# Performance work log

Measured on AMD Instinct MI355X. Metric: run time of the kernel, lower is better.

## Reference

```python
import jax, jax.numpy as jnp
import numpy as np

EPS_LN = 1e-6
NUM_HEADS = 3

def ln2d(x, w, b):
    # channels-first layernorm over dim 1 (biased variance), matching LayerNormFunction
    mu = x.mean(1, keepdims=True)
    var = ((x - mu) ** 2).mean(1, keepdims=True)
    y = (x - mu) * jax.lax.rsqrt(var + EPS_LN)
    return w[None, :, None, None] * y + b[None, :, None, None]

def conv1x1(x, w, b):
    # w: (out, in)
    return jnp.einsum('bchw,oc->bohw', x, w) + b[None, :, None, None]

def dwconv3x3(x, w, b):
    # w: (C,1,3,3), depthwise
    C = x.shape[1]
    y = jax.lax.conv_general_dilated(x, w, (1, 1), 'SAME',
        feature_group_count=C, dimension_numbers=('NCHW', 'OIHW', 'NCHW'))
    return y + b[None, :, None, None]

def l2norm(x, eps=1e-12):
    n = jnp.sqrt(jnp.sum(x * x, axis=-1, keepdims=True))
    return x / jnp.maximum(n, eps)

def forward(x, ln1_w, ln1_b, qkv_w, qkv_b, dw_w, dw_b, temp,
            ca_w1, ca_b1, ca_w2, ca_b2, beta, beta2,
            ln2_w, ln2_b, conv4_w, conv4_b, conv5_w, conv5_b, gamma):
    inp = x
    b, c, h, w = x.shape
    xn = ln2d(x, ln1_w, ln1_b)

    # CAB = SE channel attention
    y = xn.mean(axis=(2, 3), keepdims=True)                      # (b,c,1,1)
    y = jax.nn.relu(conv1x1(y, ca_w1, ca_b1))
    y = jax.nn.sigmoid(conv1x1(y, ca_w2, ca_b2))
    outc = xn * y

    # QKV
    qkv = dwconv3x3(conv1x1(xn, qkv_w, qkv_b), dw_w, dw_b)       # (b,3c,h,w)
    q, k, v = jnp.split(qkv, 3, axis=1)
    cph = c // NUM_HEADS
    def to_tokens(t):  # (b,c,h,w) -> (b,head,hw,cph)
        return t.reshape(b, NUM_HEADS, cph, h * w).transpose(0, 1, 3, 2)
    qs = l2norm(to_tokens(q))
    ks = l2norm(to_tokens(k))
    vs = to_tokens(v)

    attns = jnp.einsum('bhnc,bhmc->bhnm', qs, ks) * temp[None]   # (b,head,hw,hw)
    attns = jax.nn.softmax(jax.nn.relu(attns), axis=-1)
    outs = jnp.einsum('bhnm,bhmc->bhnc', attns, vs)              # (b,head,hw,cph)
    outs = outs.transpose(0, 1, 3, 2).reshape(b, c, h, w)

    y1 = inp + outc * beta + outs * beta2

    # gated conv FFN
    f = conv1x1(ln2d(y1, ln2_w, ln2_b), conv4_w, conv4_b)        # (b,2c,h,w)
    f1, f2 = jnp.split(f, 2, axis=1)
    f = conv1x1(f1 * f2, conv5_w, conv5_b)
    return y1 + f * gamma

def setup_inputs() -> dict:
    key = jax.random.key(0)
    ks = jax.random.split(key, 16)
    B, C, H, W = 2, 48, 64, 64
    r = C // 16
    s = 0.05
    return {
        'x': jax.random.normal(ks[0], (B, C, H, W), jnp.float32),
        'ln1_w': jnp.ones((C,), jnp.float32),
        'ln1_b': jnp.zeros((C,), jnp.float32),
        'qkv_w': jax.random.normal(ks[1], (3 * C, C), jnp.float32) * s,
        'qkv_b': jnp.zeros((3 * C,), jnp.float32),
        'dw_w': jax.random.normal(ks[2], (3 * C, 1, 3, 3), jnp.float32) * s,
        'dw_b': jnp.zeros((3 * C,), jnp.float32),
        'temp': jnp.ones((3, 1, 1), jnp.float32),
        'ca_w1': jax.random.normal(ks[3], (r, C), jnp.float32) * s,
        'ca_b1': jnp.zeros((r,), jnp.float32),
        'ca_w2': jax.random.normal(ks[4], (C, r), jnp.float32) * s,
        'ca_b2': jnp.zeros((C,), jnp.float32),
        'beta': jax.random.normal(ks[5], (1, C, 1, 1), jnp.float32) * 0.1,
        'beta2': jax.random.normal(ks[6], (1, C, 1, 1), jnp.float32) * 0.1,
        'ln2_w': jnp.ones((C,), jnp.float32),
        'ln2_b': jnp.zeros((C,), jnp.float32),
        'conv4_w': jax.random.normal(ks[7], (2 * C, C), jnp.float32) * s,
        'conv4_b': jnp.zeros((2 * C,), jnp.float32),
        'conv5_w': jax.random.normal(ks[8], (C, C), jnp.float32) * s,
        'conv5_b': jnp.zeros((C,), jnp.float32),
        'gamma': jax.random.normal(ks[9], (1, C, 1, 1), jnp.float32) * 0.1,
    }

def reference(x, ln1_w, ln1_b, qkv_w, qkv_b, dw_w, dw_b, temp,
              ca_w1, ca_b1, ca_w2, ca_b2, beta, beta2,
              ln2_w, ln2_b, conv4_w, conv4_b, conv5_w, conv5_b, gamma):
    return forward(x, ln1_w, ln1_b, qkv_w, qkv_b, dw_w, dw_b, temp,
                   ca_w1, ca_b1, ca_w2, ca_b2, beta, beta2,
                   ln2_w, ln2_b, conv4_w, conv4_b, conv5_w, conv5_b, gamma)
```

## Files before the change

kernel.cpp:

```cpp
#include <hip/hip_runtime.h>
#include <cstddef>
#include <cmath>

#define BN 2
#define CH 48
#define HW 4096
#define NH 3
#define QC 144
#define RR 3
#define KSPLIT 4
#define NPLANE 17
#define LOG2E 1.4426950408889634f

typedef __attribute__((ext_vector_type(8))) short bf16x8;
typedef __attribute__((ext_vector_type(16))) float f32x16;
typedef __attribute__((ext_vector_type(4))) float f32x4;

constexpr size_t OFF_BP  = 0;
constexpr size_t OFF_QB  = 12288;
constexpr size_t OFF_KB  = OFF_QB + 98304;
constexpr size_t OFF_VT  = OFF_KB + 98304;
constexpr size_t OFF_PART= OFF_VT + 98304 + 1179648;

static __device__ __forceinline__ unsigned cvtpk(float lo, float hi) {
  unsigned r;
  asm("v_cvt_pk_bf16_f32 %0, %1, %2" : "=v"(r) : "v"(lo), "v"(hi));
  return r;
}

static __device__ __forceinline__ float fexp2(float x) {
#if __has_builtin(__builtin_amdgcn_exp2f)
  return __builtin_amdgcn_exp2f(x);
#else
  float r; asm("v_exp_f32 %0, %1" : "=v"(r) : "v"(x)); return r;
#endif
}

__global__ __launch_bounds__(512) void k_front(const float* __restrict__ x,
                                               const float* __restrict__ lw,
                                               const float* __restrict__ lb,
                                               const float* __restrict__ w,
                                               const float* __restrict__ bias,
                                               const float* __restrict__ dww,
                                               const float* __restrict__ dwb,
                                               const float* __restrict__ temp,
                                               ushort* __restrict__ Qb,
                                               ushort* __restrict__ Kb,
                                               ushort* __restrict__ Vtb,
                                               float* __restrict__ bpool) {
  __shared__ float qt[3][CH][64];
  __shared__ float red1[8][64], red2[8][64];
  int blk = blockIdx.x;
  int row = blk & 63, bh = blk >> 6;
  int b = bh / NH, h = bh % NH;
  int t = threadIdx.x;
  int px = t & 63, grp = t >> 6;
  int lo = grp*18, hi = lo + 18;

  float xn[CH];
#pragma unroll
  for (int r = 0; r < 3; ++r) {
    int rlo = r*48, rhi = rlo + 48;
    if (lo >= rhi || hi <= rlo) continue;
    int yy = row + r - 1;
    bool oob = (yy < 0) || (yy >= 64);
    if (!oob) {
      const float* xb = x + (size_t)b*CH*HW + yy*64 + px;
      float s = 0.f, ss = 0.f;
#pragma unroll
      for (int ci = 0; ci < CH; ++ci) {
        float vv = xb[(size_t)ci*HW];
        xn[ci] = vv; s += vv; ss += vv*vv;
      }
      float mu = s * (1.f/CH);
      float rs2 = rsqrtf(ss*(1.f/CH) - mu*mu + 1e-6f);
#pragma unroll
      for (int ci = 0; ci < CH; ++ci)
        xn[ci] = lw[ci]*((xn[ci]-mu)*rs2) + lb[ci];
    }
    int ub = lo > rlo ? lo : rlo;
    int ue = hi < rhi ? hi : rhi;
    for (int u = ub; u < ue; ++u) {
      int oc = u - rlo;
      if (oob) { qt[r][oc][px] = 0.f; continue; }
      int c = __builtin_amdgcn_readfirstlane((oc >> 4)*48 + h*16 + (oc & 15));
      const float* wrow = w + (size_t)c*CH;
      float a = bias[c];
#pragma unroll
      for (int ci = 0; ci < CH; ++ci) a += wrow[ci]*xn[ci];
      qt[r][oc][px] = a;
    }
  }

  if (h == 0 && grp == 3) {
#pragma unroll
    for (int c = 0; c < CH; ++c) {
      float s = xn[c];
      s += __shfl_xor(s, 1);  s += __shfl_xor(s, 2);  s += __shfl_xor(s, 4);
      s += __shfl_xor(s, 8);  s += __shfl_xor(s, 16); s += __shfl_xor(s, 32);
      if (px == 0) bpool[(size_t)(b*64 + row)*CH + c] = s;
    }
  }
  __syncthreads();

  int n = row*64 + px;
  float q[2], k[2], vv2[2];
  float sq = 0.f, sk = 0.f;
#pragma unroll
  for (int j = 0; j < 2; ++j) {
    int cc = grp*2 + j;
#pragma unroll
    for (int which = 0; which < 3; ++which) {
      int oc = which*16 + cc;
      int cg = __builtin_amdgcn_readfirstlane(which*48 + h*16 + cc);
      const float* wc = dww + (size_t)cg*9;
      float w0 = wc[0], w1 = wc[1], w2 = wc[2],
            w3 = wc[3], w4 = wc[4], w5 = wc[5],
            w6 = wc[6], w7 = wc[7], w8 = wc[8];
      float a = dwb[cg];
#pragma unroll
      for (int rr = 0; rr < 3; ++rr) {
        float wl = rr==0?w0:(rr==1?w3:w6);
        float wm = rr==0?w1:(rr==1?w4:w7);
        float wr = rr==0?w2:(rr==1?w5:w8);
        float tm = qt[rr][oc][px];
        float tl = (px >= 1)  ? qt[rr][oc][px-1] : 0.f;
        float tr = (px <= 62) ? qt[rr][oc][px+1] : 0.f;
        a += wl*tl + wm*tm + wr*tr;
      }
      if (which == 0)      { q[j] = a;  sq += a*a; }
      else if (which == 1) { k[j] = a;  sk += a*a; }
      else                 vv2[j] = a;
    }
  }
  red1[grp][px] = sq; red2[grp][px] = sk;
  __syncthreads();
  float tsq = 0.f, tsk = 0.f;
#pragma unroll
  for (int i = 0; i < 8; ++i) { tsq += red1[i][px]; tsk += red2[i][px]; }
  float tq = temp[h] * LOG2E / fmaxf(sqrtf(tsq), 1e-12f);
  float ik = 1.f            / fmaxf(sqrtf(tsk), 1e-12f);
  *(uint*)(Qb + ((size_t)bh*HW + n)*16 + grp*2) = cvtpk(q[0]*tq, q[1]*tq);
  *(uint*)(Kb + ((size_t)bh*HW + n)*16 + grp*2) = cvtpk(k[0]*ik, k[1]*ik);
  Vtb[((size_t)bh*16 + grp*2    )*HW + n] = (ushort)(cvtpk(vv2[0], vv2[0]) & 0xffffu);
  Vtb[((size_t)bh*16 + grp*2 + 1)*HW + n] = (ushort)(cvtpk(vv2[1], vv2[1]) & 0xffffu);
}

#define PACK(stv, wbp) do {                                              \
  _Pragma("unroll")                                                      \
  for (int g4 = 0; g4 < 4; ++g4) {                                       \
    float e0 = fmaxf(fexp2((stv)[4*g4+0]), 1.f);                         \
    float e1 = fmaxf(fexp2((stv)[4*g4+1]), 1.f);                         \
    float e2 = fmaxf(fexp2((stv)[4*g4+2]), 1.f);                         \
    float e3 = fmaxf(fexp2((stv)[4*g4+3]), 1.f);                         \
    uint2 pk;                                                            \
    pk.x = cvtpk(e0, e1);                                                \
    pk.y = cvtpk(e2, e3);                                                \
    *(uint2*)((wbp) + wroff + 16*(g4 ^ sw)) = pk;                        \
  } } while (0)

__global__ __launch_bounds__(256) void k_attn(const ushort* __restrict__ Qb,
                                              const ushort* __restrict__ Kb,
                                              const ushort* __restrict__ Vtb,
                                              float* __restrict__ part) {
  __shared__ char smem[4][4096];
  int blk = blockIdx.x;
  int ks = blk & (KSPLIT-1);
  int qt = (blk >> 2) & 31;
  int bh = blk >> 7;
  int lane = threadIdx.x & 63;
  int wid  = threadIdx.x >> 6;
  int l31 = lane & 31;
  int lhi = lane >> 5;
  int qbase = qt*128 + wid*32;

  bf16x8 qf = *(const bf16x8*)(Qb + ((size_t)bh*HW + qbase + l31)*16 + lhi*8);

  const f32x16 z16 = {0,0,0,0,0,0,0,0,0,0,0,0,0,0,0,0};
  const short oneb = (short)0x3f80;
  const bf16x8 ones = {oneb,oneb,oneb,oneb,oneb,oneb,oneb,oneb};
  f32x4 acc0 = {0,0,0,0}, acc1 = {0,0,0,0};
  f32x4 accD0 = {0,0,0,0}, accD1 = {0,0,0,0};
  char* base = &smem[wid][0];
  int qr = lane & 15, gr = lane >> 4;
  int rdoff0 = qr*64 + 16*(gr ^ ((qr>>1)&3));
  int sw = (l31 >> 1) & 3;
  int wroff = l31*64 + 8*lhi;

  const ushort* Kbase = Kb + (size_t)bh*HW*16;
  const ushort* Vbase = Vtb + ((size_t)bh*16 + qr)*HW;
  int kbeg = ks * (HW/KSPLIT);
  constexpr int ITERS = (HW/KSPLIT)/32;

  bf16x8 kf = *(const bf16x8*)(Kbase + (size_t)(kbeg + l31)*16 + lhi*8);
  f32x16 st = __builtin_amdgcn_mfma_f32_32x32x16_bf16(kf, qf, z16, 0, 0, 0);
  bf16x8 kfn = *(const bf16x8*)(Kbase + (size_t)(kbeg + 32 + l31)*16 + lhi*8);
  bf16x8 vfn = *(const bf16x8*)(Vbase + kbeg + 8*gr);
  PACK(st, base);

#pragma unroll 4
  for (int i = 1; i < ITERS; ++i) {
    char* rb = base + ((i-1) & 1)*2048;
    bf16x8 pa0 = *(const bf16x8*)(rb + rdoff0);
    bf16x8 pa1 = *(const bf16x8*)(rb + 1024 + rdoff0);
    __builtin_amdgcn_s_setprio(1);
    f32x16 stn = __builtin_amdgcn_mfma_f32_32x32x16_bf16(kfn, qf, z16, 0, 0, 0);
    kfn = *(const bf16x8*)(Kbase + (size_t)(kbeg + (i+1)*32 + l31)*16 + lhi*8);
    bf16x8 vf = vfn;
    vfn = *(const bf16x8*)(Vbase + kbeg + i*32 + 8*gr);
    acc0  = __builtin_amdgcn_mfma_f32_16x16x32_bf16(pa0, vf, acc0, 0, 0, 0);
    acc1  = __builtin_amdgcn_mfma_f32_16x16x32_bf16(pa1, vf, acc1, 0, 0, 0);
    accD0 = __builtin_amdgcn_mfma_f32_16x16x32_bf16(pa0, ones, accD0, 0, 0, 0);
    accD1 = __builtin_amdgcn_mfma_f32_16x16x32_bf16(pa1, ones, accD1, 0, 0, 0);
    __builtin_amdgcn_s_setprio(0);
    PACK(stn, base + (i & 1)*2048);
  }
  {
    char* rb = base + ((ITERS-1) & 1)*2048;
    bf16x8 pa0 = *(const bf16x8*)(rb + rdoff0);
    bf16x8 pa1 = *(const bf16x8*)(rb + 1024 + rdoff0);
    acc0  = __builtin_amdgcn_mfma_f32_16x16x32_bf16(pa0, vfn, acc0, 0, 0, 0);
    acc1  = __builtin_amdgcn_mfma_f32_16x16x32_bf16(pa1, vfn, acc1, 0, 0, 0);
    accD0 = __builtin_amdgcn_mfma_f32_16x16x32_bf16(pa0, ones, accD0, 0, 0, 0);
    accD1 = __builtin_amdgcn_mfma_f32_16x16x32_bf16(pa1, ones, accD1, 0, 0, 0);
  }

  float* ep = (float*)base;
#pragma unroll
  for (int r = 0; r < 4; ++r) {
    ep[qr*32 + gr*4 + r]      = acc0[r];
    ep[qr*32 + gr*4 + 16 + r] = acc1[r];
  }
  if (qr == 0) {
#pragma unroll
    for (int r = 0; r < 4; ++r) {
      ep[16*32 + gr*4 + r]      = accD0[r];
      ep[16*32 + gr*4 + 16 + r] = accD1[r];
    }
  }
  __syncthreads();
  size_t pb = ((size_t)(ks*6 + bh))*NPLANE;
  for (int i = threadIdx.x; i < 4*32*NPLANE; i += 256) {
    int w = i / (32*NPLANE);
    int rem = i - w*(32*NPLANE);
    int cc = rem >> 5;
    int q = rem & 31;
    part[(pb + cc)*HW + qt*128 + w*32 + q] = ((float*)&smem[w][0])[cc*32 + q];
  }
}

__global__ __launch_bounds__(768) void k_tail(const float* __restrict__ part,
                                              const float* __restrict__ x,
                                              const float* __restrict__ lw1,
                                              const float* __restrict__ lb1,
                                              const float* __restrict__ bpool,
                                              const float* __restrict__ w1,
                                              const float* __restrict__ b1,
                                              const float* __restrict__ w2,
                                              const float* __restrict__ b2,
                                              const float* __restrict__ beta,
                                              const float* __restrict__ beta2,
                                              const float* __restrict__ lw2,
                                              const float* __restrict__ lb2,
                                              const float* __restrict__ w4,
                                              const float* __restrict__ b4,
                                              const float* __restrict__ w5,
                                              const float* __restrict__ b5,
                                              const float* __restrict__ gamma,
                                              float* __restrict__ out) {
  __shared__ float sepm[CH][4];
  __shared__ float pmL[CH];
  __shared__ float yrL[4];
  __shared__ float seL[CH];
  __shared__ float r1[12][64], r2[12][64], r3[12][64], r4[12][64];
  __shared__ float xt[CH][65];
  __shared__ float gt[CH][65];
  int t = threadIdx.x;
  int px = t & 63, w = t >> 6;
  int h = w >> 2;
  int c0 = __builtin_amdgcn_readfirstlane(w * 4);
  int qoff = __builtin_amdgcn_readfirstlane((w & 3) * 4);
  int gp = blockIdx.x*64 + px;
  int b = gp >> 12, n = gp & 4095;
  int bh = b*NH + h;

  if (t < 192) {
    int c = t % CH, j = t / CH;
    const float* bp = bpool + (size_t)(b*64 + j*16)*CH + c;
    float a = 0.f;
#pragma unroll
    for (int i = 0; i < 16; ++i) a += bp[(size_t)i*CH];
    sepm[c][j] = a;
  }
  __syncthreads();
  if (t < CH) pmL[t] = (sepm[t][0]+sepm[t][1]+sepm[t][2]+sepm[t][3]) * (1.f/HW);
  __syncthreads();
  if (t < RR) {
    float a = b1[t];
    for (int c = 0; c < CH; ++c) a += w1[t*CH+c]*pmL[c];
    yrL[t] = fmaxf(a, 0.f);
  }
  __syncthreads();
  if (t < CH) {
    float a = b2[t];
    for (int r = 0; r < RR; ++r) a += w2[t*RR+r]*yrL[r];
    seL[t] = 1.f/(1.f+__expf(-a));
  }

  float acc[4] = {0,0,0,0};
  float den = 0.f;
#pragma unroll
  for (int ks = 0; ks < KSPLIT; ++ks) {
    const float* pl = part + ((size_t)((ks*6+bh)*NPLANE + qoff))*HW + n;
#pragma unroll
    for (int cc = 0; cc < 4; ++cc) acc[cc] += pl[(size_t)cc*HW];
    den += pl[(size_t)(16 - qoff)*HW];
  }
  const float* xp = x + ((size_t)b*CH + c0)*HW + n;
  float xv[4]; float s = 0.f, ssum = 0.f;
#pragma unroll
  for (int cc = 0; cc < 4; ++cc) {
    float vv = xp[(size_t)cc*HW];
    xv[cc] = vv; s += vv; ssum += vv*vv;
  }
  r1[w][px] = s; r2[w][px] = ssum;
  __syncthreads();
  float stot = 0.f, sstot = 0.f;
#pragma unroll
  for (int i = 0; i < 12; ++i) { stot += r1[i][px]; sstot += r2[i][px]; }
  float mu = stot*(1.f/CH);
  float rs = rsqrtf(sstot*(1.f/CH) - mu*mu + 1e-6f);
  float inv = 1.f / den;
  float yv[4]; float s2 = 0.f, ss2 = 0.f;
#pragma unroll
  for (int cc = 0; cc < 4; ++cc) {
    int c = c0 + cc;
    float xnv = lw1[c]*((xv[cc]-mu)*rs) + lb1[c];
    float y = xv[cc] + xnv*seL[c]*beta[c] + acc[cc]*inv*beta2[c];
    yv[cc] = y; s2 += y; ss2 += y*y;
  }
  r3[w][px] = s2; r4[w][px] = ss2;
  __syncthreads();
  float s2t = 0.f, ss2t = 0.f;
#pragma unroll
  for (int i = 0; i < 12; ++i) { s2t += r3[i][px]; ss2t += r4[i][px]; }
  float mu2 = s2t*(1.f/CH);
  float rs2 = rsqrtf(ss2t*(1.f/CH) - mu2*mu2 + 1e-6f);
#pragma unroll
  for (int cc = 0; cc < 4; ++cc) {
    int c = c0 + cc;
    xt[c][px] = lw2[c]*((yv[cc]-mu2)*rs2) + lb2[c];
  }
  __syncthreads();

  float f1[4], f2[4];
#pragma unroll
  for (int j = 0; j < 4; ++j) { f1[j] = b4[c0+j]; f2[j] = b4[CH+c0+j]; }
#pragma unroll 8
  for (int c = 0; c < CH; ++c) {
    float tc = xt[c][px];
#pragma unroll
    for (int j = 0; j < 4; ++j) {
      f1[j] += w4[(size_t)(c0+j)*CH + c] * tc;
      f2[j] += w4[(size_t)(CH+c0+j)*CH + c] * tc;
    }
  }
#pragma unroll
  for (int j = 0; j < 4; ++j) gt[c0+j][px] = f1[j]*f2[j];
  __syncthreads();

  float f5[4];
#pragma unroll
  for (int j = 0; j < 4; ++j) f5[j] = b5[c0+j];
#pragma unroll 8
  for (int c = 0; c < CH; ++c) {
    float gc = gt[c][px];
#pragma unroll
    for (int j = 0; j < 4; ++j) f5[j] += w5[(size_t)(c0+j)*CH + c] * gc;
  }
  float* op = out + ((size_t)b*CH + c0)*HW + n;
#pragma unroll
  for (int j = 0; j < 4; ++j)
    op[(size_t)j*HW] = yv[j] + f5[j]*gamma[c0+j];
}

extern "C" void kernel_launch(void* const* d_in, const int* in_sizes, int n_in,
                              void* d_out, int out_size, void* d_ws, size_t ws_size,
                              hipStream_t stream) {
  const float* x      = (const float*)d_in[0];
  const float* ln1_w  = (const float*)d_in[1];
  const float* ln1_b  = (const float*)d_in[2];
  const float* qkv_w  = (const float*)d_in[3];
  const float* qkv_b  = (const float*)d_in[4];
  const float* dw_w   = (const float*)d_in[5];
  const float* dw_b   = (const float*)d_in[6];
  const float* temp   = (const float*)d_in[7];
  const float* ca_w1  = (const float*)d_in[8];
  const float* ca_b1  = (const float*)d_in[9];
  const float* ca_w2  = (const float*)d_in[10];
  const float* ca_b2  = (const float*)d_in[11];
  const float* beta   = (const float*)d_in[12];
  const float* beta2  = (const float*)d_in[13];
  const float* ln2_w  = (const float*)d_in[14];
  const float* ln2_b  = (const float*)d_in[15];
  const float* conv4_w= (const float*)d_in[16];
  const float* conv4_b= (const float*)d_in[17];
  const float* conv5_w= (const float*)d_in[18];
  const float* conv5_b= (const float*)d_in[19];
  const float* gamma  = (const float*)d_in[20];

  float* ws   = (float*)d_ws;
  float* bp   = ws + OFF_BP;
  ushort* Qb  = (ushort*)(ws + OFF_QB);
  ushort* Kb  = (ushort*)(ws + OFF_KB);
  ushort* Vtb = (ushort*)(ws + OFF_VT);
  float* part = ws + OFF_PART;
  float* out  = (float*)d_out;

  k_front<<<384, 512, 0, stream>>>(x, ln1_w, ln1_b, qkv_w, qkv_b,
                                   dw_w, dw_b, temp, Qb, Kb, Vtb, bp);
  k_attn <<<768, 256, 0, stream>>>(Qb, Kb, Vtb, part);
  k_tail <<<128, 768, 0, stream>>>(part, x, ln1_w, ln1_b, bp,
                                   ca_w1, ca_b1, ca_w2, ca_b2,
                                   beta, beta2, ln2_w, ln2_b,
                                   conv4_w, conv4_b, conv5_w, conv5_b,
                                   gamma, out);
}
```

Baseline: 60.32 us.

## Stage normalized input rows in LDS and compute per-thread qkv channels with shuffle-based dwconv

Restructures the front kernel. Only three waves now load and layer-normalize the three input rows, storing them channel-last in shared memory. Each wave then computes the 1x1 conv for exactly the six channels it needs in the depthwise stage, keeping the results in registers and taking horizontal neighbours through wave shuffles instead of a shared qkv tile. This removes the uneven 18-channel split and the qkv LDS round trip. In exchange, each thread recomputes three rows of 1x1 conv outputs and holds a larger register array.

```diff
diff --git a/kernel.cpp b/kernel.cpp
--- a/kernel.cpp
+++ b/kernel.cpp
@@ -48,90 +48,93 @@
                                                ushort* __restrict__ Kb,
                                                ushort* __restrict__ Vtb,
                                                float* __restrict__ bpool) {
-  __shared__ float qt[3][CH][64];
+  __shared__ float xt3[3][64][CH];
   __shared__ float red1[8][64], red2[8][64];
   int blk = blockIdx.x;
   int row = blk & 63, bh = blk >> 6;
   int b = bh / NH, h = bh % NH;
   int t = threadIdx.x;
   int px = t & 63, grp = t >> 6;
-  int lo = grp*18, hi = lo + 18;
-
-  float xn[CH];
-#pragma unroll
-  for (int r = 0; r < 3; ++r) {
-    int rlo = r*48, rhi = rlo + 48;
-    if (lo >= rhi || hi <= rlo) continue;
-    int yy = row + r - 1;
-    bool oob = (yy < 0) || (yy >= 64);
-    if (!oob) {
+
+  if (grp < 3) {
+    int yy = row + grp - 1;
+    if (yy >= 0 && yy < 64) {
       const float* xb = x + (size_t)b*CH*HW + yy*64 + px;
-      float s = 0.f, ss = 0.f;
+      float xn[CH]; float s = 0.f, ss = 0.f;
 #pragma unroll
       for (int ci = 0; ci < CH; ++ci) {
         float vv = xb[(size_t)ci*HW];
         xn[ci] = vv; s += vv; ss += vv*vv;
       }
       float mu = s * (1.f/CH);
-      float rs2 = rsqrtf(ss*(1.f/CH) - mu*mu + 1e-6f);
+      float rs = rsqrtf(ss*(1.f/CH) - mu*mu + 1e-6f);
 #pragma unroll
       for (int ci = 0; ci < CH; ++ci)
-        xn[ci] = lw[ci]*((xn[ci]-mu)*rs2) + lb[ci];
-    }
-    int ub = lo > rlo ? lo : rlo;
-    int ue = hi < rhi ? hi : rhi;
-    for (int u = ub; u < ue; ++u) {
-      int oc = u - rlo;
-      if (oob) { qt[r][oc][px] = 0.f; continue; }
-      int c = __builtin_amdgcn_readfirstlane((oc >> 4)*48 + h*16 + (oc & 15));
+        xn[ci] = lw[ci]*((xn[ci]-mu)*rs) + lb[ci];
+#pragma unroll
+      for (int c4 = 0; c4 < CH/4; ++c4)
+        *(float4*)&xt3[grp][px][c4*4] =
+          make_float4(xn[c4*4], xn[c4*4+1], xn[c4*4+2], xn[c4*4+3]);
+      if (h == 0 && grp == 1) {
+#pragma unroll
+        for (int c = 0; c < CH; ++c) {
+          float s2 = xn[c];
+          s2 += __shfl_xor(s2, 1);  s2 += __shfl_xor(s2, 2);
+          s2 += __shfl_xor(s2, 4);  s2 += __shfl_xor(s2, 8);
+          s2 += __shfl_xor(s2, 16); s2 += __shfl_xor(s2, 32);
+          if (px == 0) bpool[(size_t)(b*64 + row)*CH + c] = s2;
+        }
+      }
+    }
+  }
+  __syncthreads();
+
+  float qtr[6][3];
+#pragma unroll
+  for (int r = 0; r < 3; ++r) {
+    int yy = row + r - 1;
+    if (yy < 0 || yy >= 64) {
+#pragma unroll
+      for (int i = 0; i < 6; ++i) qtr[i][r] = 0.f;
+      continue;
+    }
+    float xv[CH];
+#pragma unroll
+    for (int c4 = 0; c4 < CH/4; ++c4) {
+      float4 v4 = *(float4*)&xt3[r][px][c4*4];
+      xv[c4*4] = v4.x; xv[c4*4+1] = v4.y; xv[c4*4+2] = v4.z; xv[c4*4+3] = v4.w;
+    }
+#pragma unroll
+    for (int i = 0; i < 6; ++i) {
+      int which = i >> 1, cc = grp*2 + (i & 1);
+      int c = __builtin_amdgcn_readfirstlane(which*48 + h*16 + cc);
       const float* wrow = w + (size_t)c*CH;
       float a = bias[c];
 #pragma unroll
-      for (int ci = 0; ci < CH; ++ci) a += wrow[ci]*xn[ci];
-      qt[r][oc][px] = a;
-    }
-  }
-
-  if (h == 0 && grp == 3) {
-#pragma unroll
-    for (int c = 0; c < CH; ++c) {
-      float s = xn[c];
-      s += __shfl_xor(s, 1);  s += __shfl_xor(s, 2);  s += __shfl_xor(s, 4);
-      s += __shfl_xor(s, 8);  s += __shfl_xor(s, 16); s += __shfl_xor(s, 32);
-      if (px == 0) bpool[(size_t)(b*64 + row)*CH + c] = s;
-    }
-  }
-  __syncthreads();
+      for (int ci = 0; ci < CH; ++ci) a += wrow[ci]*xv[ci];
+      qtr[i][r] = a;
+    }
+  }
 
   int n = row*64 + px;
   float q[2], k[2], vv2[2];
   float sq = 0.f, sk = 0.f;
 #pragma unroll
-  for (int j = 0; j < 2; ++j) {
-    int cc = grp*2 + j;
-#pragma unroll
-    for (int which = 0; which < 3; ++which) {
-      int oc = which*16 + cc;
-      int cg = __builtin_amdgcn_readfirstlane(which*48 + h*16 + cc);
-      const float* wc = dww + (size_t)cg*9;
-      float w0 = wc[0], w1 = wc[1], w2 = wc[2],
-            w3 = wc[3], w4 = wc[4], w5 = wc[5],
-            w6 = wc[6], w7 = wc[7], w8 = wc[8];
-      float a = dwb[cg];
-#pragma unroll
-      for (int rr = 0; rr < 3; ++rr) {
-        float wl = rr==0?w0:(rr==1?w3:w6);
-        float wm = rr==0?w1:(rr==1?w4:w7);
-        float wr = rr==0?w2:(rr==1?w5:w8);
-        float tm = qt[rr][oc][px];
-        float tl = (px >= 1)  ? qt[rr][oc][px-1] : 0.f;
-        float tr = (px <= 62) ? qt[rr][oc][px+1] : 0.f;
-        a += wl*tl + wm*tm + wr*tr;
-      }
-      if (which == 0)      { q[j] = a;  sq += a*a; }
-      else if (which == 1) { k[j] = a;  sk += a*a; }
-      else                 vv2[j] = a;
-    }
+  for (int i = 0; i < 6; ++i) {
+    int which = i >> 1, j = i & 1, cc = grp*2 + j;
+    int cg = __builtin_amdgcn_readfirstlane(which*48 + h*16 + cc);
+    const float* wc = dww + (size_t)cg*9;
+    float a = dwb[cg];
+#pragma unroll
+    for (int rr = 0; rr < 3; ++rr) {
+      float tm = qtr[i][rr];
+      float tl = __shfl(tm, px - 1); tl = (px >= 1)  ? tl : 0.f;
+      float tr = __shfl(tm, px + 1); tr = (px <= 62) ? tr : 0.f;
+      a += wc[rr*3]*tl + wc[rr*3+1]*tm + wc[rr*3+2]*tr;
+    }
+    if (which == 0)      { q[j] = a;  sq += a*a; }
+    else if (which == 1) { k[j] = a;  sk += a*a; }
+    else                 vv2[j] = a;
   }
   red1[grp][px] = sq; red2[grp][px] = sk;
   __syncthreads();
```

After: 61.53 us. 2.0% more time.
